# Kernel optimization log

Hardware: AMD Instinct MI355X
Metric: run time of the kernel (lower is better)

## Reference

```python
import jax, jax.numpy as jnp
import numpy as np
from jax import lax

B_SZ, C_IN, T_LEN = 8, 80, 1000
D_MODEL, D_STATE, D_CONV, EXPAND = 256, 16, 4, 2
D_INNER = EXPAND * D_MODEL
DT_RANK = D_MODEL // 16  # math.ceil(256/16) = 16
N_LABELS = 35


def setup_inputs() -> dict:
    key = jax.random.key(0)
    ks = jax.random.split(key, 12)
    s = lambda k, shape: (jax.random.normal(k, shape, jnp.float32) * 0.02)
    A_log = jnp.log(jnp.tile(jnp.arange(1, D_STATE + 1, dtype=jnp.float32), (D_INNER, 1)))
    return {
        "x": jax.random.normal(ks[0], (B_SZ, C_IN, T_LEN), jnp.float32),
        "proj_w": s(ks[1], (D_MODEL, C_IN)),
        "proj_b": jnp.zeros((D_MODEL,), jnp.float32),
        "in_proj_w": s(ks[2], (2 * D_INNER, D_MODEL)),
        "conv_w": s(ks[3], (D_INNER, D_CONV)),
        "conv_b": jnp.zeros((D_INNER,), jnp.float32),
        "x_proj_w": s(ks[4], (DT_RANK + 2 * D_STATE, D_INNER)),
        "dt_proj_w": s(ks[5], (D_INNER, DT_RANK)),
        "dt_proj_b": jax.random.uniform(ks[6], (D_INNER,), jnp.float32, -4.0, -2.0),
        "A_log": A_log,
        "D": jnp.ones((D_INNER,), jnp.float32),
        "out_proj_w": s(ks[7], (D_MODEL, D_INNER)),
        "fc_w": s(ks[8], (N_LABELS, D_MODEL)),
        "fc_b": jnp.zeros((N_LABELS,), jnp.float32),
    }


def _mamba(u, in_proj_w, conv_w, conv_b, x_proj_w, dt_proj_w, dt_proj_b, A_log, D, out_proj_w):
    # u: (B, L, d_model) -> (B, L, d_model)
    Bn, L, _ = u.shape
    xz = u @ in_proj_w.T                      # (B, L, 2*d_inner)
    xh, z = jnp.split(xz, 2, axis=-1)
    # causal depthwise conv along L
    xc = jnp.pad(xh.transpose(0, 2, 1), ((0, 0), (0, 0), (D_CONV - 1, 0)))  # (B, d_inner, L+pad)
    xh = lax.conv_general_dilated(xc, conv_w[:, None, :], (1,), 'VALID',
                                  feature_group_count=D_INNER)             # (B, d_inner, L)
    xh = jax.nn.silu(xh.transpose(0, 2, 1) + conv_b)                        # (B, L, d_inner)
    dbc = xh @ x_proj_w.T                                                   # (B, L, dt_rank+2*d_state)
    dt, Bm, Cm = jnp.split(dbc, [DT_RANK, DT_RANK + D_STATE], axis=-1)
    delta = jax.nn.softplus(dt @ dt_proj_w.T + dt_proj_b)                   # (B, L, d_inner)
    A = -jnp.exp(A_log)                                                     # (d_inner, d_state)
    deltaA = jnp.exp(delta[..., None] * A)                                  # (B, L, d_inner, d_state)
    deltaBu = delta[..., None] * Bm[:, :, None, :] * xh[..., None]          # (B, L, d_inner, d_state)

    def step(h, inp):
        dA_t, dBu_t, C_t = inp
        h = dA_t * h + dBu_t                    # (B, d_inner, d_state)
        y_t = jnp.einsum('bds,bs->bd', h, C_t)  # (B, d_inner)
        return h, y_t

    h0 = jnp.zeros((Bn, D_INNER, D_STATE), u.dtype)
    _, ys = lax.scan(step, h0,
                     (deltaA.transpose(1, 0, 2, 3),
                      deltaBu.transpose(1, 0, 2, 3),
                      Cm.transpose(1, 0, 2)))
    y = ys.transpose(1, 0, 2) + xh * D          # (B, L, d_inner)
    y = y * jax.nn.silu(z)
    return y @ out_proj_w.T                     # (B, L, d_model)


def reference(x, proj_w, proj_b, in_proj_w, conv_w, conv_b, x_proj_w,
              dt_proj_w, dt_proj_b, A_log, D, out_proj_w, fc_w, fc_b):
    # x: (B, input_dim, T) -> permute -> Linear -> (B, T, d_model)
    h = x.transpose(0, 2, 1) @ proj_w.T + proj_b
    # Mamba selective scan over the time axis (model permutes channel-first; math identical)
    y = _mamba(h, in_proj_w, conv_w, conv_b, x_proj_w, dt_proj_w, dt_proj_b,
               A_log, D, out_proj_w)            # (B, T, d_model)
    # dropout is identity at inference; mean over time (== mean(dim=2) on (B,d_model,T))
    pooled = y.mean(axis=1)                     # (B, d_model)
    return pooled @ fc_w.T + fc_b               # (B, n_labels)
```

## Files before the change

### kernel.cpp

```cpp
#include <hip/hip_runtime.h>
#include <math.h>


#define OFF_W1T   0
#define OFF_B1    81920
#define OFF_W2S   82944
#define OFF_AL2   100864
#define OFF_XH    109056
#define OFF_SZ    4205056
#define OFF_PACK  8301056
#define OFF_BC    16493056
#define OFF_CHUNK 16749056
#define OFF_DBCP  OFF_CHUNK
#define OFF_YBAR  18878976
#define WS_FLOATS 18883072

#define CK_FLOATS 262144
#define CHUNK_BASE(ck) ((ck) < 8 ? (OFF_XH + (ck) * CK_FLOATS) \
                                 : (OFF_CHUNK + ((ck) - 8) * CK_FLOATS))
#define OFF_ACC16 (OFF_XH + 2097152)

__device__ __forceinline__ float silu_f(float v) {
  return v / (1.f + __expf(-v));
}

__global__ __launch_bounds__(256) void prep_w1t(const float* __restrict__ proj_w,
                                                const float* __restrict__ in_proj_w,
                                                float* __restrict__ ws) {
  const int nt = blockIdx.x;
  const int ct = blockIdx.y;
  const int n0 = nt * 64, c0 = ct * 16;
  __shared__ float Pl[16 * 68];
  __shared__ float Il[64 * 68];
  const int tid = threadIdx.x;
  const int ng = tid & 31, cg = tid >> 5;
  float acc[2][2] = {{0.f, 0.f}, {0.f, 0.f}};
  for (int kc = 0; kc < 256; kc += 64) {
    __syncthreads();
    for (int i = tid; i < 16 * 64; i += 256) {
      int k = i >> 4, c = i & 15;
      Pl[c * 68 + k] = proj_w[(kc + k) * 80 + c0 + c];
    }
    for (int i = tid; i < 64 * 64; i += 256) {
      int n = i >> 6, k = i & 63;
      Il[k * 68 + n] = in_proj_w[(n0 + n) * 256 + kc + k];
    }
    __syncthreads();
    for (int k = 0; k < 64; ++k) {
      float p0 = Pl[(cg * 2 + 0) * 68 + k];
      float p1 = Pl[(cg * 2 + 1) * 68 + k];
      float2 iv = *(const float2*)&Il[k * 68 + ng * 2];
      acc[0][0] = fmaf(p0, iv.x, acc[0][0]);
      acc[0][1] = fmaf(p0, iv.y, acc[0][1]);
      acc[1][0] = fmaf(p1, iv.x, acc[1][0]);
      acc[1][1] = fmaf(p1, iv.y, acc[1][1]);
    }
  }
  for (int r = 0; r < 2; ++r)
    for (int q = 0; q < 2; ++q)
      ws[OFF_W1T + (c0 + cg * 2 + r) * 1024 + n0 + ng * 2 + q] = acc[r][q];
}

__global__ __launch_bounds__(256) void prep_small(const float* __restrict__ proj_b,
                                                  const float* __restrict__ in_proj_w,
                                                  const float* __restrict__ fc_w,
                                                  const float* __restrict__ out_proj_w,
                                                  const float* __restrict__ A_log,
                                                  float* __restrict__ ws) {
  int idx = blockIdx.x * 256 + threadIdx.x;
  if (idx < 1024) {
    float s = 0.f;
    for (int m = 0; m < 256; ++m) s = fmaf(in_proj_w[idx * 256 + m], proj_b[m], s);
    ws[OFF_B1 + idx] = s;
  } else if (idx < 1024 + 17920) {
    int j = idx - 1024;
    int n = j / 512, d = j - n * 512;
    float s = 0.f;
    for (int m = 0; m < 256; ++m) s = fmaf(fc_w[n * 256 + m], out_proj_w[m * 512 + d], s);
    ws[OFF_W2S + j] = s * 1e-3f;
  } else if (idx < 1024 + 17920 + 8192) {
    int j = idx - (1024 + 17920);
    ws[OFF_AL2 + j] = -expf(A_log[j]);
  }
}

__global__ __launch_bounds__(256) void k1_xz(const float* __restrict__ x,
                                             const float* __restrict__ conv_w,
                                             const float* __restrict__ conv_b,
                                             float* __restrict__ ws) {
  const int nt  = blockIdx.x;
  const int tch = blockIdx.y;
  const int b   = blockIdx.z;
  const int tid = threadIdx.x;
  const int n = nt * 256 + tid;
  const int t0 = tch * 16;
  const int tbase = t0 - 4;

  __shared__ __align__(16) float xs[80 * 20];
  for (int i = tid; i < 1600; i += 256) {
    int k = i / 20, j = i - k * 20;
    int t = tbase + j;
    float v = 0.f;
    if (t >= 0 && t < 1000) v = x[(b * 80 + k) * 1000 + t];
    xs[i] = v;
  }
  __syncthreads();

  float acc[20];
  {
    const float b1v = ws[OFF_B1 + n];
#pragma unroll
    for (int j = 0; j < 20; ++j) acc[j] = b1v;
  }

  const float* __restrict__ w1t = ws + OFF_W1T;
  for (int kc = 0; kc < 80; kc += 8) {
    float wreg[8];
#pragma unroll
    for (int kk = 0; kk < 8; ++kk)
      wreg[kk] = w1t[(kc + kk) * 1024 + n];
#pragma unroll
    for (int kk = 0; kk < 8; ++kk) {
      const float w = wreg[kk];
      const float* xr = &xs[(kc + kk) * 20];
#pragma unroll
      for (int g = 0; g < 5; ++g) {
        float4 xv = *(const float4*)(xr + g * 4);
        acc[g * 4 + 0] = fmaf(xv.x, w, acc[g * 4 + 0]);
        acc[g * 4 + 1] = fmaf(xv.y, w, acc[g * 4 + 1]);
        acc[g * 4 + 2] = fmaf(xv.z, w, acc[g * 4 + 2]);
        acc[g * 4 + 3] = fmaf(xv.w, w, acc[g * 4 + 3]);
      }
    }
  }

  if (tch == 0) {
    acc[0] = 0.f; acc[1] = 0.f; acc[2] = 0.f; acc[3] = 0.f;
  }

  if (nt < 2) {
    const int d = n;
    const float4 cw = *(const float4*)&conv_w[d * 4];
    const float cb = conv_b[d];
#pragma unroll
    for (int i = 0; i < 16; ++i) {
      int t = t0 + i;
      if (t < 1000) {
        float v = cb;
        v = fmaf(cw.x, acc[i + 1], v);
        v = fmaf(cw.y, acc[i + 2], v);
        v = fmaf(cw.z, acc[i + 3], v);
        v = fmaf(cw.w, acc[i + 4], v);
        ws[OFF_XH + (b * 1000 + t) * 512 + d] = silu_f(v);
      }
    }
  } else {
    const int d0 = n - 512;
#pragma unroll
    for (int i = 0; i < 16; ++i) {
      int t = t0 + i;
      if (t < 1000)
        ws[OFF_SZ + (b * 1000 + t) * 512 + d0] = silu_f(acc[i + 4]);
    }
  }
}

__global__ __launch_bounds__(256) void k2b_dbc(const float* __restrict__ x_proj_w,
                                               float* __restrict__ ws) {
  const int row0 = blockIdx.x * 16;
  const int ks   = blockIdx.y;
  const int k0   = ks * 256;
  __shared__ float Xl[16 * 68];
  __shared__ float Wl[48 * 68];
  const int tid = threadIdx.x;
  const int ng = tid & 15, rg = tid >> 4;
  float acc[3] = {0.f, 0.f, 0.f};
  for (int kc = 0; kc < 256; kc += 64) {
    __syncthreads();
    for (int i = tid; i < 16 * 64; i += 256) {
      int r = i >> 6, c = i & 63;
      Xl[r * 68 + c] = ws[OFF_XH + (row0 + r) * 512 + k0 + kc + c];
    }
    for (int i = tid; i < 48 * 64; i += 256) {
      int r = i >> 6, c = i & 63;
      Wl[r * 68 + c] = x_proj_w[r * 512 + k0 + kc + c];
    }
    __syncthreads();
    for (int c = 0; c < 64; c += 4) {
      float4 xa = *(const float4*)&Xl[rg * 68 + c];
      float4 w0 = *(const float4*)&Wl[(ng * 3 + 0) * 68 + c];
      float4 w1 = *(const float4*)&Wl[(ng * 3 + 1) * 68 + c];
      float4 w2 = *(const float4*)&Wl[(ng * 3 + 2) * 68 + c];
      acc[0] += xa.x*w0.x + xa.y*w0.y + xa.z*w0.z + xa.w*w0.w;
      acc[1] += xa.x*w1.x + xa.y*w1.y + xa.z*w1.z + xa.w*w1.w;
      acc[2] += xa.x*w2.x + xa.y*w2.y + xa.z*w2.z + xa.w*w2.w;
    }
  }
  for (int n = 0; n < 3; ++n)
    ws[OFF_DBCP + ks * 384000 + (row0 + rg) * 48 + ng * 3 + n] = acc[n];
}

__global__ __launch_bounds__(256) void k2c_pack(const float* __restrict__ dt_proj_w,
                                                const float* __restrict__ dt_proj_b,
                                                float* __restrict__ ws) {
  const int tb = blockIdx.x;
  const int b  = blockIdx.y;
  const int tid = threadIdx.x;
  __shared__ float dbcl[8 * 48];
  for (int i = tid; i < 8 * 48; i += 256) {
    int tt = i / 48, c = i - tt * 48;
    int row = b * 1000 + tb * 8 + tt;
    dbcl[i] = ws[OFF_DBCP + row * 48 + c] + ws[OFF_DBCP + 384000 + row * 48 + c];
  }
  __syncthreads();
  if (tid < 128) {
    int tt = tid >> 4, s = tid & 15;
    int row = b * 1000 + tb * 8 + tt;
    *(float2*)&ws[OFF_BC + (row * 16 + s) * 2] =
        make_float2(dbcl[tt * 48 + 16 + s], dbcl[tt * 48 + 32 + s]);
  }
  for (int dd = tid; dd < 512; dd += 256) {
    const float4* wp = (const float4*)(dt_proj_w + dd * 16);
    float4 w0 = wp[0], w1 = wp[1], w2 = wp[2], w3 = wp[3];
    float bias = dt_proj_b[dd];
#pragma unroll
    for (int tt = 0; tt < 8; ++tt) {
      int row = b * 1000 + tb * 8 + tt;
      const float* dr = &dbcl[tt * 48];
      float lin = bias;
      lin = fmaf(dr[0],  w0.x, lin); lin = fmaf(dr[1],  w0.y, lin);
      lin = fmaf(dr[2],  w0.z, lin); lin = fmaf(dr[3],  w0.w, lin);
      lin = fmaf(dr[4],  w1.x, lin); lin = fmaf(dr[5],  w1.y, lin);
      lin = fmaf(dr[6],  w1.z, lin); lin = fmaf(dr[7],  w1.w, lin);
      lin = fmaf(dr[8],  w2.x, lin); lin = fmaf(dr[9],  w2.y, lin);
      lin = fmaf(dr[10], w2.z, lin); lin = fmaf(dr[11], w2.w, lin);
      lin = fmaf(dr[12], w3.x, lin); lin = fmaf(dr[13], w3.y, lin);
      lin = fmaf(dr[14], w3.z, lin); lin = fmaf(dr[15], w3.w, lin);
      float delta = fmaxf(lin, 0.f) + log1pf(__expf(-fabsf(lin)));
      float xh = ws[OFF_XH + row * 512 + dd];
      *(float2*)&ws[OFF_PACK + (row * 512 + dd) * 2] = make_float2(delta, xh);
    }
  }
}

__global__ __launch_bounds__(512) void k3_scan1(float* __restrict__ ws) {
  const int dg = blockIdx.x;
  const int ck = blockIdx.y;
  const int b  = blockIdx.z;
  const int tid = threadIdx.x;
  const int lane = tid & 63;
  const int wv = tid >> 6;
  const int d = dg * 64 + lane;
  const float2 av = *(const float2*)&ws[OFF_AL2 + d * 16 + wv * 2];
  const float a0 = av.x, a1 = av.y;
  const int nt = (ck < 8) ? 63 : 62;
  const int tstart = (ck < 8) ? 63 * ck : 62 * ck + 8;
  const int rowbase = b * 1000 + tstart;
  __shared__ __align__(16) float bcl[63 * 32];
  for (int i = tid; i < nt * 32; i += 512) bcl[i] = ws[OFF_BC + rowbase * 32 + i];
  __syncthreads();
  const float2* __restrict__ packp = (const float2*)(ws + OFF_PACK) + rowbase * 512 + d;
  const float*  __restrict__ szp   = ws + OFF_SZ + rowbase * 512 + d;
  float h0 = 0.f, h1 = 0.f, cp0 = 1.f, cp1 = 1.f;
  float S10 = 0.f, S11 = 0.f, S20 = 0.f, S21 = 0.f, xacc = 0.f;
#pragma unroll 4
  for (int i = 0; i < nt; ++i) {
    float2 p  = packp[i * 512];
    float sz  = szp[i * 512];
    float4 bc = *(const float4*)&bcl[i * 32 + wv * 4];
    float du = p.x * p.y;
    xacc = fmaf(p.y, sz, xacc);
    float e0 = __expf(p.x * a0), e1 = __expf(p.x * a1);
    cp0 *= e0; cp1 *= e1;
    h0 = fmaf(e0, h0, du * bc.x);
    h1 = fmaf(e1, h1, du * bc.z);
    float cs0 = bc.y * sz, cs1 = bc.w * sz;
    S10 = fmaf(h0, cs0, S10); S11 = fmaf(h1, cs1, S11);
    S20 = fmaf(cp0, cs0, S20); S21 = fmaf(cp1, cs1, S21);
  }
  {
    const int cbase = CHUNK_BASE(ck);
    const int s = wv * 2;
    int idx = (b * 16 + s) * 512 + d;
    *(float4*)&ws[cbase + idx * 4] = make_float4(cp0, h0, S10, S20);
    *(float4*)&ws[cbase + (idx + 512) * 4] = make_float4(cp1, h1, S11, S21);
  }
  if (wv == 0) ws[OFF_ACC16 + (ck * 8 + b) * 512 + d] = xacc;
}

__global__ __launch_bounds__(256) void k4_scan2(const float* __restrict__ Dvec,
                                                float* __restrict__ ws) {
  const int dg = blockIdx.x;
  const int b  = blockIdx.y;
  const int tid = threadIdx.x;
  const int dl = tid & 15, s = tid >> 4;
  const int d = dg * 16 + dl;
  const int lane = tid & 63, wv = tid >> 6;
  float h = 0.f, y = 0.f;
#pragma unroll
  for (int k = 0; k < 16; ++k) {
    const float4 f = *(const float4*)&ws[CHUNK_BASE(k) + ((b * 16 + s) * 512 + d) * 4];
    y = fmaf(f.w, h, y + f.z);
    h = fmaf(f.x, h, f.y);
  }
  y += __shfl_xor(y, 16);
  y += __shfl_xor(y, 32);
  __shared__ float ys[4][16];
  if (lane < 16) ys[wv][dl] = y;
  __syncthreads();
  if (tid < 16) {
    float yt = ys[0][tid] + ys[1][tid] + ys[2][tid] + ys[3][tid];
    float acc = 0.f;
#pragma unroll
    for (int k = 0; k < 16; ++k) acc += ws[OFF_ACC16 + (k * 8 + b) * 512 + dg * 16 + tid];
    int dd = dg * 16 + tid;
    ws[OFF_YBAR + b * 512 + dd] = yt + Dvec[dd] * acc;
  }
}

__global__ __launch_bounds__(64) void k5_out(const float* __restrict__ fc_b,
                                             const float* __restrict__ ws,
                                             float* __restrict__ out) {
  const int b = blockIdx.x;
  const int n = threadIdx.x;
  if (n >= 35) return;
  const float* yb = ws + OFF_YBAR + b * 512;
  const float* w  = ws + OFF_W2S + n * 512;
  float sum = 0.f;
#pragma unroll 8
  for (int k = 0; k < 512; ++k) sum = fmaf(yb[k], w[k], sum);
  out[b * 35 + n] = sum + fc_b[n];
}

extern "C" void kernel_launch(void* const* d_in, const int* in_sizes, int n_in,
                              void* d_out, int out_size, void* d_ws, size_t ws_size,
                              hipStream_t stream) {
  const float* x          = (const float*)d_in[0];
  const float* proj_w     = (const float*)d_in[1];
  const float* proj_b     = (const float*)d_in[2];
  const float* in_proj_w  = (const float*)d_in[3];
  const float* conv_w     = (const float*)d_in[4];
  const float* conv_b     = (const float*)d_in[5];
  const float* x_proj_w   = (const float*)d_in[6];
  const float* dt_proj_w  = (const float*)d_in[7];
  const float* dt_proj_b  = (const float*)d_in[8];
  const float* A_log      = (const float*)d_in[9];
  const float* Dvec       = (const float*)d_in[10];
  const float* out_proj_w = (const float*)d_in[11];
  const float* fc_w       = (const float*)d_in[12];
  const float* fc_b       = (const float*)d_in[13];
  float* ws  = (float*)d_ws;
  float* out = (float*)d_out;
  if (ws_size < (size_t)WS_FLOATS * sizeof(float)) return;

  prep_w1t  <<<dim3(16, 5),    256, 0, stream>>>(proj_w, in_proj_w, ws);
  prep_small<<<106,            256, 0, stream>>>(proj_b, in_proj_w, fc_w, out_proj_w, A_log, ws);
  k1_xz     <<<dim3(4, 63, 8), 256, 0, stream>>>(x, conv_w, conv_b, ws);
  k2b_dbc   <<<dim3(500, 2),   256, 0, stream>>>(x_proj_w, ws);
  k2c_pack  <<<dim3(125, 8),   256, 0, stream>>>(dt_proj_w, dt_proj_b, ws);
  k3_scan1  <<<dim3(8, 16, 8), 512, 0, stream>>>(ws);
  k4_scan2  <<<dim3(32, 8),    256, 0, stream>>>(Dvec, ws);
  k5_out    <<<8,              64,  0, stream>>>(fc_b, ws, out);
}
```

Measured before the change: 164.1 us.

## Register-tile k1_xz GEMM as 8 channels x 12 timesteps per thread

Restructures the input-projection kernel so each thread computes 8 output channels across 12 timesteps (8 outputs plus a 4-step halo), with each wave of the block handling a different 8-step time window. This replaces the earlier one-channel-by-20-timestep tile, raising arithmetic intensity per weight and per shared-memory load and halving the grid. The cost is a 96-float accumulator array, which increases register pressure and lowers occupancy, and halo recomputation now happens per wave rather than per block.

```diff
diff --git a/kernel.cpp b/kernel.cpp
--- a/kernel.cpp
+++ b/kernel.cpp
@@ -89,78 +89,87 @@
                                              const float* __restrict__ conv_b,
                                              float* __restrict__ ws) {
   const int nt  = blockIdx.x;
-  const int tch = blockIdx.y;
+  const int tcb = blockIdx.y;
   const int b   = blockIdx.z;
   const int tid = threadIdx.x;
-  const int n = nt * 256 + tid;
-  const int t0 = tch * 16;
-  const int tbase = t0 - 4;
-
-  __shared__ __align__(16) float xs[80 * 20];
-  for (int i = tid; i < 1600; i += 256) {
-    int k = i / 20, j = i - k * 20;
-    int t = tbase + j;
+  const int lane = tid & 63;
+  const int wv   = tid >> 6;
+  const int t0b  = tcb * 32;
+  const int tw0  = t0b + wv * 8;
+
+  __shared__ __align__(16) float xs[80 * 36];
+  for (int i = tid; i < 2880; i += 256) {
+    int k = i / 36, j = i - k * 36;
+    int t = t0b - 4 + j;
     float v = 0.f;
     if (t >= 0 && t < 1000) v = x[(b * 80 + k) * 1000 + t];
     xs[i] = v;
   }
   __syncthreads();
 
-  float acc[20];
-  {
-    const float b1v = ws[OFF_B1 + n];
-#pragma unroll
-    for (int j = 0; j < 20; ++j) acc[j] = b1v;
+  const int nb = nt * 512 + lane;
+  float acc[8][12];
+#pragma unroll
+  for (int c = 0; c < 8; ++c) {
+    float b1v = ws[OFF_B1 + nb + 64 * c];
+#pragma unroll
+    for (int j = 0; j < 12; ++j) acc[c][j] = b1v;
   }
 
   const float* __restrict__ w1t = ws + OFF_W1T;
-  for (int kc = 0; kc < 80; kc += 8) {
+  const int woff = wv * 8;
+  for (int k = 0; k < 80; ++k) {
     float wreg[8];
 #pragma unroll
-    for (int kk = 0; kk < 8; ++kk)
-      wreg[kk] = w1t[(kc + kk) * 1024 + n];
-#pragma unroll
-    for (int kk = 0; kk < 8; ++kk) {
-      const float w = wreg[kk];
-      const float* xr = &xs[(kc + kk) * 20];
-#pragma unroll
-      for (int g = 0; g < 5; ++g) {
-        float4 xv = *(const float4*)(xr + g * 4);
-        acc[g * 4 + 0] = fmaf(xv.x, w, acc[g * 4 + 0]);
-        acc[g * 4 + 1] = fmaf(xv.y, w, acc[g * 4 + 1]);
-        acc[g * 4 + 2] = fmaf(xv.z, w, acc[g * 4 + 2]);
-        acc[g * 4 + 3] = fmaf(xv.w, w, acc[g * 4 + 3]);
+    for (int c = 0; c < 8; ++c)
+      wreg[c] = w1t[k * 1024 + nb + 64 * c];
+    float xv[12];
+    *(float4*)&xv[0] = *(const float4*)&xs[k * 36 + woff + 0];
+    *(float4*)&xv[4] = *(const float4*)&xs[k * 36 + woff + 4];
+    *(float4*)&xv[8] = *(const float4*)&xs[k * 36 + woff + 8];
+#pragma unroll
+    for (int c = 0; c < 8; ++c)
+#pragma unroll
+      for (int j = 0; j < 12; ++j)
+        acc[c][j] = fmaf(xv[j], wreg[c], acc[c][j]);
+  }
+
+  if (tcb == 0 && wv == 0) {
+#pragma unroll
+    for (int c = 0; c < 8; ++c) {
+      acc[c][0] = 0.f; acc[c][1] = 0.f; acc[c][2] = 0.f; acc[c][3] = 0.f;
+    }
+  }
+
+  if (nt == 0) {
+#pragma unroll
+    for (int c = 0; c < 8; ++c) {
+      const int d = nb + 64 * c;
+      const float4 cw = *(const float4*)&conv_w[d * 4];
+      const float cb = conv_b[d];
+#pragma unroll
+      for (int i = 0; i < 8; ++i) {
+        int t = tw0 + i;
+        if (t < 1000) {
+          float v = cb;
+          v = fmaf(cw.x, acc[c][i + 1], v);
+          v = fmaf(cw.y, acc[c][i + 2], v);
+          v = fmaf(cw.z, acc[c][i + 3], v);
+          v = fmaf(cw.w, acc[c][i + 4], v);
+          ws[OFF_XH + (b * 1000 + t) * 512 + d] = silu_f(v);
+        }
       }
     }
-  }
-
-  if (tch == 0) {
-    acc[0] = 0.f; acc[1] = 0.f; acc[2] = 0.f; acc[3] = 0.f;
-  }
-
-  if (nt < 2) {
-    const int d = n;
-    const float4 cw = *(const float4*)&conv_w[d * 4];
-    const float cb = conv_b[d];
-#pragma unroll
-    for (int i = 0; i < 16; ++i) {
-      int t = t0 + i;
-      if (t < 1000) {
-        float v = cb;
-        v = fmaf(cw.x, acc[i + 1], v);
-        v = fmaf(cw.y, acc[i + 2], v);
-        v = fmaf(cw.z, acc[i + 3], v);
-        v = fmaf(cw.w, acc[i + 4], v);
-        ws[OFF_XH + (b * 1000 + t) * 512 + d] = silu_f(v);
+  } else {
+#pragma unroll
+    for (int c = 0; c < 8; ++c) {
+      const int d0 = lane + 64 * c;
+#pragma unroll
+      for (int i = 0; i < 8; ++i) {
+        int t = tw0 + i;
+        if (t < 1000)
+          ws[OFF_SZ + (b * 1000 + t) * 512 + d0] = silu_f(acc[c][i + 4]);
       }
-    }
-  } else {
-    const int d0 = n - 512;
-#pragma unroll
-    for (int i = 0; i < 16; ++i) {
-      int t = t0 + i;
-      if (t < 1000)
-        ws[OFF_SZ + (b * 1000 + t) * 512 + d0] = silu_f(acc[i + 4]);
     }
   }
 }
@@ -355,7 +364,7 @@
 
   prep_w1t  <<<dim3(16, 5),    256, 0, stream>>>(proj_w, in_proj_w, ws);
   prep_small<<<106,            256, 0, stream>>>(proj_b, in_proj_w, fc_w, out_proj_w, A_log, ws);
-  k1_xz     <<<dim3(4, 63, 8), 256, 0, stream>>>(x, conv_w, conv_b, ws);
+  k1_xz     <<<dim3(2, 32, 8), 256, 0, stream>>>(x, conv_w, conv_b, ws);
   k2b_dbc   <<<dim3(500, 2),   256, 0, stream>>>(x_proj_w, ws);
   k2c_pack  <<<dim3(125, 8),   256, 0, stream>>>(dt_proj_w, dt_proj_b, ws);
   k3_scan1  <<<dim3(8, 16, 8), 512, 0, stream>>>(ws);
```

Measured after the change: 175.7 us. 1.07x slower.

## Fuse delta computation into chunked scan and merge prep kernels

Applied to the files above, without the earlier changes.

Removes the separate pack kernel: the scan kernel now sums the split-K x_proj partials into shared memory, computes softplus(dt) per chunk in shared memory, and reads xh directly instead of a packed (delta, xh) buffer. It also re-chunks the time axis into 20 chunks of 50 steps, with k4 adjusted to match, and merges the two prep kernels into one launch. The goal is to cut global traffic for the packed buffer and to save launches. The cost is redundant dt_proj work across d-groups and extra shared memory in the scan kernel.

```diff
diff --git a/kernel.cpp b/kernel.cpp
--- a/kernel.cpp
+++ b/kernel.cpp
@@ -2,85 +2,82 @@
 #include <math.h>
 
 
-#define OFF_W1T   0
-#define OFF_B1    81920
-#define OFF_W2S   82944
-#define OFF_AL2   100864
-#define OFF_XH    109056
-#define OFF_SZ    4205056
-#define OFF_PACK  8301056
-#define OFF_BC    16493056
-#define OFF_CHUNK 16749056
-#define OFF_DBCP  OFF_CHUNK
-#define OFF_YBAR  18878976
-#define WS_FLOATS 18883072
+#define OFF_W1T    0
+#define OFF_B1     81920
+#define OFF_W2S    82944
+#define OFF_AL2    100864
+#define OFF_XH     109056
+#define OFF_SZ     4205056
+#define OFF_CHUNKA 8301056
+#define OFF_ACC20  13543936
+#define OFF_DBCP   13625856
+#define OFF_YBAR   18878976
+#define WS_FLOATS  18883072
 
 #define CK_FLOATS 262144
-#define CHUNK_BASE(ck) ((ck) < 8 ? (OFF_XH + (ck) * CK_FLOATS) \
-                                 : (OFF_CHUNK + ((ck) - 8) * CK_FLOATS))
-#define OFF_ACC16 (OFF_XH + 2097152)
+#define CHUNK_BASE(ck) (OFF_CHUNKA + (ck) * CK_FLOATS)
+#define K3_NT 50
 
 __device__ __forceinline__ float silu_f(float v) {
   return v / (1.f + __expf(-v));
 }
 
-__global__ __launch_bounds__(256) void prep_w1t(const float* __restrict__ proj_w,
+__global__ __launch_bounds__(256) void prep_all(const float* __restrict__ proj_w,
+                                                const float* __restrict__ proj_b,
                                                 const float* __restrict__ in_proj_w,
+                                                const float* __restrict__ fc_w,
+                                                const float* __restrict__ out_proj_w,
+                                                const float* __restrict__ A_log,
                                                 float* __restrict__ ws) {
-  const int nt = blockIdx.x;
-  const int ct = blockIdx.y;
-  const int n0 = nt * 64, c0 = ct * 16;
-  __shared__ float Pl[16 * 68];
-  __shared__ float Il[64 * 68];
-  const int tid = threadIdx.x;
-  const int ng = tid & 31, cg = tid >> 5;
-  float acc[2][2] = {{0.f, 0.f}, {0.f, 0.f}};
-  for (int kc = 0; kc < 256; kc += 64) {
-    __syncthreads();
-    for (int i = tid; i < 16 * 64; i += 256) {
-      int k = i >> 4, c = i & 15;
-      Pl[c * 68 + k] = proj_w[(kc + k) * 80 + c0 + c];
-    }
-    for (int i = tid; i < 64 * 64; i += 256) {
-      int n = i >> 6, k = i & 63;
-      Il[k * 68 + n] = in_proj_w[(n0 + n) * 256 + kc + k];
-    }
-    __syncthreads();
-    for (int k = 0; k < 64; ++k) {
-      float p0 = Pl[(cg * 2 + 0) * 68 + k];
-      float p1 = Pl[(cg * 2 + 1) * 68 + k];
-      float2 iv = *(const float2*)&Il[k * 68 + ng * 2];
-      acc[0][0] = fmaf(p0, iv.x, acc[0][0]);
-      acc[0][1] = fmaf(p0, iv.y, acc[0][1]);
-      acc[1][0] = fmaf(p1, iv.x, acc[1][0]);
-      acc[1][1] = fmaf(p1, iv.y, acc[1][1]);
-    }
-  }
-  for (int r = 0; r < 2; ++r)
-    for (int q = 0; q < 2; ++q)
-      ws[OFF_W1T + (c0 + cg * 2 + r) * 1024 + n0 + ng * 2 + q] = acc[r][q];
-}
-
-__global__ __launch_bounds__(256) void prep_small(const float* __restrict__ proj_b,
-                                                  const float* __restrict__ in_proj_w,
-                                                  const float* __restrict__ fc_w,
-                                                  const float* __restrict__ out_proj_w,
-                                                  const float* __restrict__ A_log,
-                                                  float* __restrict__ ws) {
-  int idx = blockIdx.x * 256 + threadIdx.x;
-  if (idx < 1024) {
-    float s = 0.f;
-    for (int m = 0; m < 256; ++m) s = fmaf(in_proj_w[idx * 256 + m], proj_b[m], s);
-    ws[OFF_B1 + idx] = s;
-  } else if (idx < 1024 + 17920) {
-    int j = idx - 1024;
-    int n = j / 512, d = j - n * 512;
-    float s = 0.f;
-    for (int m = 0; m < 256; ++m) s = fmaf(fc_w[n * 256 + m], out_proj_w[m * 512 + d], s);
-    ws[OFF_W2S + j] = s * 1e-3f;
-  } else if (idx < 1024 + 17920 + 8192) {
-    int j = idx - (1024 + 17920);
-    ws[OFF_AL2 + j] = -expf(A_log[j]);
+  const int tid = threadIdx.x;
+  if (blockIdx.x < 80) {
+    const int nt = blockIdx.x / 5;
+    const int ct = blockIdx.x % 5;
+    const int n0 = nt * 64, c0 = ct * 16;
+    __shared__ float Pl[16 * 68];
+    __shared__ float Il[64 * 68];
+    const int ng = tid & 31, cg = tid >> 5;
+    float acc[2][2] = {{0.f, 0.f}, {0.f, 0.f}};
+    for (int kc = 0; kc < 256; kc += 64) {
+      __syncthreads();
+      for (int i = tid; i < 16 * 64; i += 256) {
+        int k = i >> 4, c = i & 15;
+        Pl[c * 68 + k] = proj_w[(kc + k) * 80 + c0 + c];
+      }
+      for (int i = tid; i < 64 * 64; i += 256) {
+        int n = i >> 6, k = i & 63;
+        Il[k * 68 + n] = in_proj_w[(n0 + n) * 256 + kc + k];
+      }
+      __syncthreads();
+      for (int k = 0; k < 64; ++k) {
+        float p0 = Pl[(cg * 2 + 0) * 68 + k];
+        float p1 = Pl[(cg * 2 + 1) * 68 + k];
+        float2 iv = *(const float2*)&Il[k * 68 + ng * 2];
+        acc[0][0] = fmaf(p0, iv.x, acc[0][0]);
+        acc[0][1] = fmaf(p0, iv.y, acc[0][1]);
+        acc[1][0] = fmaf(p1, iv.x, acc[1][0]);
+        acc[1][1] = fmaf(p1, iv.y, acc[1][1]);
+      }
+    }
+    for (int r = 0; r < 2; ++r)
+      for (int q = 0; q < 2; ++q)
+        ws[OFF_W1T + (c0 + cg * 2 + r) * 1024 + n0 + ng * 2 + q] = acc[r][q];
+  } else {
+    int idx = (blockIdx.x - 80) * 256 + tid;
+    if (idx < 1024) {
+      float s = 0.f;
+      for (int m = 0; m < 256; ++m) s = fmaf(in_proj_w[idx * 256 + m], proj_b[m], s);
+      ws[OFF_B1 + idx] = s;
+    } else if (idx < 1024 + 17920) {
+      int j = idx - 1024;
+      int n = j / 512, d = j - n * 512;
+      float s = 0.f;
+      for (int m = 0; m < 256; ++m) s = fmaf(fc_w[n * 256 + m], out_proj_w[m * 512 + d], s);
+      ws[OFF_W2S + j] = s * 1e-3f;
+    } else if (idx < 1024 + 17920 + 8192) {
+      int j = idx - (1024 + 17920);
+      ws[OFF_AL2 + j] = -expf(A_log[j]);
+    }
   }
 }
 
@@ -200,50 +197,9 @@
     ws[OFF_DBCP + ks * 384000 + (row0 + rg) * 48 + ng * 3 + n] = acc[n];
 }
 
-__global__ __launch_bounds__(256) void k2c_pack(const float* __restrict__ dt_proj_w,
+__global__ __launch_bounds__(512) void k3_scan1(const float* __restrict__ dt_proj_w,
                                                 const float* __restrict__ dt_proj_b,
                                                 float* __restrict__ ws) {
-  const int tb = blockIdx.x;
-  const int b  = blockIdx.y;
-  const int tid = threadIdx.x;
-  __shared__ float dbcl[8 * 48];
-  for (int i = tid; i < 8 * 48; i += 256) {
-    int tt = i / 48, c = i - tt * 48;
-    int row = b * 1000 + tb * 8 + tt;
-    dbcl[i] = ws[OFF_DBCP + row * 48 + c] + ws[OFF_DBCP + 384000 + row * 48 + c];
-  }
-  __syncthreads();
-  if (tid < 128) {
-    int tt = tid >> 4, s = tid & 15;
-    int row = b * 1000 + tb * 8 + tt;
-    *(float2*)&ws[OFF_BC + (row * 16 + s) * 2] =
-        make_float2(dbcl[tt * 48 + 16 + s], dbcl[tt * 48 + 32 + s]);
-  }
-  for (int dd = tid; dd < 512; dd += 256) {
-    const float4* wp = (const float4*)(dt_proj_w + dd * 16);
-    float4 w0 = wp[0], w1 = wp[1], w2 = wp[2], w3 = wp[3];
-    float bias = dt_proj_b[dd];
-#pragma unroll
-    for (int tt = 0; tt < 8; ++tt) {
-      int row = b * 1000 + tb * 8 + tt;
-      const float* dr = &dbcl[tt * 48];
-      float lin = bias;
-      lin = fmaf(dr[0],  w0.x, lin); lin = fmaf(dr[1],  w0.y, lin);
-      lin = fmaf(dr[2],  w0.z, lin); lin = fmaf(dr[3],  w0.w, lin);
-      lin = fmaf(dr[4],  w1.x, lin); lin = fmaf(dr[5],  w1.y, lin);
-      lin = fmaf(dr[6],  w1.z, lin); lin = fmaf(dr[7],  w1.w, lin);
-      lin = fmaf(dr[8],  w2.x, lin); lin = fmaf(dr[9],  w2.y, lin);
-      lin = fmaf(dr[10], w2.z, lin); lin = fmaf(dr[11], w2.w, lin);
-      lin = fmaf(dr[12], w3.x, lin); lin = fmaf(dr[13], w3.y, lin);
-      lin = fmaf(dr[14], w3.z, lin); lin = fmaf(dr[15], w3.w, lin);
-      float delta = fmaxf(lin, 0.f) + log1pf(__expf(-fabsf(lin)));
-      float xh = ws[OFF_XH + row * 512 + dd];
-      *(float2*)&ws[OFF_PACK + (row * 512 + dd) * 2] = make_float2(delta, xh);
-    }
-  }
-}
-
-__global__ __launch_bounds__(512) void k3_scan1(float* __restrict__ ws) {
   const int dg = blockIdx.x;
   const int ck = blockIdx.y;
   const int b  = blockIdx.z;
@@ -251,30 +207,59 @@
   const int lane = tid & 63;
   const int wv = tid >> 6;
   const int d = dg * 64 + lane;
+  const int rowbase = b * 1000 + ck * K3_NT;
+
+  __shared__ __align__(16) float dbcl[K3_NT * 48];
+  __shared__ float dlt[K3_NT * 64];
+  for (int i = tid; i < K3_NT * 48; i += 512)
+    dbcl[i] = ws[OFF_DBCP + rowbase * 48 + i] +
+              ws[OFF_DBCP + 384000 + rowbase * 48 + i];
+  __syncthreads();
+
+  {
+    const float4* wp = (const float4*)(dt_proj_w + d * 16);
+    const float4 w0 = wp[0], w1 = wp[1], w2 = wp[2], w3 = wp[3];
+    const float bias = dt_proj_b[d];
+    for (int tt = wv; tt < K3_NT; tt += 8) {
+      const float* dr = &dbcl[tt * 48];
+      float4 q0 = *(const float4*)(dr + 0);
+      float4 q1 = *(const float4*)(dr + 4);
+      float4 q2 = *(const float4*)(dr + 8);
+      float4 q3 = *(const float4*)(dr + 12);
+      float lin = bias;
+      lin = fmaf(q0.x, w0.x, lin); lin = fmaf(q0.y, w0.y, lin);
+      lin = fmaf(q0.z, w0.z, lin); lin = fmaf(q0.w, w0.w, lin);
+      lin = fmaf(q1.x, w1.x, lin); lin = fmaf(q1.y, w1.y, lin);
+      lin = fmaf(q1.z, w1.z, lin); lin = fmaf(q1.w, w1.w, lin);
+      lin = fmaf(q2.x, w2.x, lin); lin = fmaf(q2.y, w2.y, lin);
+      lin = fmaf(q2.z, w2.z, lin); lin = fmaf(q2.w, w2.w, lin);
+      lin = fmaf(q3.x, w3.x, lin); lin = fmaf(q3.y, w3.y, lin);
+      lin = fmaf(q3.z, w3.z, lin); lin = fmaf(q3.w, w3.w, lin);
+      dlt[tt * 64 + lane] = fmaxf(lin, 0.f) + log1pf(__expf(-fabsf(lin)));
+    }
+  }
+  __syncthreads();
+
   const float2 av = *(const float2*)&ws[OFF_AL2 + d * 16 + wv * 2];
   const float a0 = av.x, a1 = av.y;
-  const int nt = (ck < 8) ? 63 : 62;
-  const int tstart = (ck < 8) ? 63 * ck : 62 * ck + 8;
-  const int rowbase = b * 1000 + tstart;
-  __shared__ __align__(16) float bcl[63 * 32];
-  for (int i = tid; i < nt * 32; i += 512) bcl[i] = ws[OFF_BC + rowbase * 32 + i];
-  __syncthreads();
-  const float2* __restrict__ packp = (const float2*)(ws + OFF_PACK) + rowbase * 512 + d;
-  const float*  __restrict__ szp   = ws + OFF_SZ + rowbase * 512 + d;
+  const float* __restrict__ xhp = ws + OFF_XH + rowbase * 512 + d;
+  const float* __restrict__ szp = ws + OFF_SZ + rowbase * 512 + d;
   float h0 = 0.f, h1 = 0.f, cp0 = 1.f, cp1 = 1.f;
   float S10 = 0.f, S11 = 0.f, S20 = 0.f, S21 = 0.f, xacc = 0.f;
-#pragma unroll 4
-  for (int i = 0; i < nt; ++i) {
-    float2 p  = packp[i * 512];
+#pragma unroll 5
+  for (int i = 0; i < K3_NT; ++i) {
+    float del = dlt[i * 64 + lane];
+    float xh  = xhp[i * 512];
     float sz  = szp[i * 512];
-    float4 bc = *(const float4*)&bcl[i * 32 + wv * 4];
-    float du = p.x * p.y;
-    xacc = fmaf(p.y, sz, xacc);
-    float e0 = __expf(p.x * a0), e1 = __expf(p.x * a1);
+    float2 bB = *(const float2*)&dbcl[i * 48 + 16 + wv * 2];
+    float2 bC = *(const float2*)&dbcl[i * 48 + 32 + wv * 2];
+    float du = del * xh;
+    xacc = fmaf(xh, sz, xacc);
+    float e0 = __expf(del * a0), e1 = __expf(del * a1);
     cp0 *= e0; cp1 *= e1;
-    h0 = fmaf(e0, h0, du * bc.x);
-    h1 = fmaf(e1, h1, du * bc.z);
-    float cs0 = bc.y * sz, cs1 = bc.w * sz;
+    h0 = fmaf(e0, h0, du * bB.x);
+    h1 = fmaf(e1, h1, du * bB.y);
+    float cs0 = bC.x * sz, cs1 = bC.y * sz;
     S10 = fmaf(h0, cs0, S10); S11 = fmaf(h1, cs1, S11);
     S20 = fmaf(cp0, cs0, S20); S21 = fmaf(cp1, cs1, S21);
   }
@@ -285,7 +270,7 @@
     *(float4*)&ws[cbase + idx * 4] = make_float4(cp0, h0, S10, S20);
     *(float4*)&ws[cbase + (idx + 512) * 4] = make_float4(cp1, h1, S11, S21);
   }
-  if (wv == 0) ws[OFF_ACC16 + (ck * 8 + b) * 512 + d] = xacc;
+  if (wv == 0) ws[OFF_ACC20 + (ck * 8 + b) * 512 + d] = xacc;
 }
 
 __global__ __launch_bounds__(256) void k4_scan2(const float* __restrict__ Dvec,
@@ -298,7 +283,7 @@
   const int lane = tid & 63, wv = tid >> 6;
   float h = 0.f, y = 0.f;
 #pragma unroll
-  for (int k = 0; k < 16; ++k) {
+  for (int k = 0; k < 20; ++k) {
     const float4 f = *(const float4*)&ws[CHUNK_BASE(k) + ((b * 16 + s) * 512 + d) * 4];
     y = fmaf(f.w, h, y + f.z);
     h = fmaf(f.x, h, f.y);
@@ -312,7 +297,7 @@
     float yt = ys[0][tid] + ys[1][tid] + ys[2][tid] + ys[3][tid];
     float acc = 0.f;
 #pragma unroll
-    for (int k = 0; k < 16; ++k) acc += ws[OFF_ACC16 + (k * 8 + b) * 512 + dg * 16 + tid];
+    for (int k = 0; k < 20; ++k) acc += ws[OFF_ACC20 + (k * 8 + b) * 512 + dg * 16 + tid];
     int dd = dg * 16 + tid;
     ws[OFF_YBAR + b * 512 + dd] = yt + Dvec[dd] * acc;
   }
@@ -353,12 +338,11 @@
   float* out = (float*)d_out;
   if (ws_size < (size_t)WS_FLOATS * sizeof(float)) return;
 
-  prep_w1t  <<<dim3(16, 5),    256, 0, stream>>>(proj_w, in_proj_w, ws);
-  prep_small<<<106,            256, 0, stream>>>(proj_b, in_proj_w, fc_w, out_proj_w, A_log, ws);
-  k1_xz     <<<dim3(4, 63, 8), 256, 0, stream>>>(x, conv_w, conv_b, ws);
-  k2b_dbc   <<<dim3(500, 2),   256, 0, stream>>>(x_proj_w, ws);
-  k2c_pack  <<<dim3(125, 8),   256, 0, stream>>>(dt_proj_w, dt_proj_b, ws);
-  k3_scan1  <<<dim3(8, 16, 8), 512, 0, stream>>>(ws);
-  k4_scan2  <<<dim3(32, 8),    256, 0, stream>>>(Dvec, ws);
-  k5_out    <<<8,              64,  0, stream>>>(fc_b, ws, out);
-}
+  prep_all  <<<186,             256, 0, stream>>>(proj_w, proj_b, in_proj_w, fc_w,
+                                                  out_proj_w, A_log, ws);
+  k1_xz     <<<dim3(4, 63, 8),  256, 0, stream>>>(x, conv_w, conv_b, ws);
+  k2b_dbc   <<<dim3(500, 2),    256, 0, stream>>>(x_proj_w, ws);
+  k3_scan1  <<<dim3(8, 20, 8),  512, 0, stream>>>(dt_proj_w, dt_proj_b, ws);
+  k4_scan2  <<<dim3(32, 8),     256, 0, stream>>>(Dvec, ws);
+  k5_out    <<<8,               64,  0, stream>>>(fc_b, ws, out);
+}
```

Result: faster. 139.9 us (-14.8%).
